# Optimization experiments

Measured on AMD Instinct MI355X. Metric: run time of the kernel, lower is better.

## Reference

```python
import jax, jax.numpy as jnp
import numpy as np

NUM_EXPERTS = 8
K = 2
N_EMBD = 1024
HIDDEN = 4 * N_EMBD
BATCH = 2
SEQ = 1024
LB_SCALE = 0.01
NOISY_STD = 1.0
INIT_S = 0.02


def setup_inputs() -> dict:
    key = jax.random.key(0)
    ks = jax.random.split(key, 8)
    D, H, E = N_EMBD, HIDDEN, NUM_EXPERTS
    return {
        "x": jax.random.normal(ks[0], (BATCH, SEQ, D), jnp.float32),
        "noise": jax.random.normal(ks[1], (BATCH, SEQ, E), jnp.float32),  # torch.randn_like(logits)
        "gate_w": jax.random.normal(ks[2], (E, D), jnp.float32) * INIT_S,
        "noise_weight": jnp.zeros((E,), jnp.float32),  # initialized to zeros in the module
        "w1": jax.random.normal(ks[3], (E, H, D), jnp.float32) * INIT_S,
        "b1": jnp.zeros((E, H), jnp.float32),
        "w2": jax.random.normal(ks[4], (E, H, D), jnp.float32) * INIT_S,
        "b2": jnp.zeros((E, H), jnp.float32),
        "wp": jax.random.normal(ks[5], (E, D, H), jnp.float32) * INIT_S,
        "bp": jnp.zeros((E, D), jnp.float32),
    }


def reference(x, noise, gate_w, noise_weight, w1, b1, w2, b2, wp, bp):
    B, S, D = x.shape
    E = gate_w.shape[0]

    # ---- TopKGateParallel ----
    logits = jnp.einsum('bsd,ed->bse', x, gate_w)           # [B,S,E]
    gate_weights = jax.nn.softmax(logits, axis=-1)
    gw_mean = gate_weights.reshape(-1, E).mean(axis=0)       # [E]
    load_balance_loss = jnp.mean((gw_mean - 1.0 / E) ** 2) * LB_SCALE  # mse vs uniform

    logits_noisy = logits + (noise * NOISY_STD) * noise_weight
    top_v, top_i = jax.lax.top_k(logits_noisy, K)            # [B,S,K]
    # scatter top-k logits into a -inf sea, then softmax -> zeros at non-topk slots
    topk_mask = jnp.sum(jax.nn.one_hot(top_i, E, dtype=jnp.float32), axis=-2) > 0  # [B,S,E]
    sparse_logits = jnp.where(topk_mask, logits_noisy, -jnp.inf)
    top_k_gated_weights = jax.nn.softmax(sparse_logits, axis=-1)  # [B,S,E]

    # ---- expert compute + weighted combine (world_size=1: all experts local) ----
    x_flat = x.reshape(B * S, D)                              # [T,D]
    w_flat = top_k_gated_weights.reshape(B * S, E)            # [T,E]
    y = jnp.zeros_like(x_flat)
    for e in range(E):  # fixed small set of experts
        h = x_flat @ w1[e].T + b1[e]                          # [T,H]
        g = x_flat @ w2[e].T + b2[e]                          # [T,H]
        out_e = (h * jax.nn.silu(g)) @ wp[e].T + bp[e]        # [T,D]
        y = y + w_flat[:, e:e + 1] * out_e
    y = y.reshape(B, S, D)
    return y, load_balance_loss
```

## Files before the change

kernel.cpp:

```cpp
#include <hip/hip_runtime.h>

#define TOK 2048
#define DIM 1024
#define HID 4096
#define NE 8
#define KSPLIT 4
#define TMAX 24

typedef unsigned short u16;
typedef __attribute__((ext_vector_type(8))) short s16x8;
typedef __attribute__((ext_vector_type(4))) float f32x4;

__device__ __forceinline__ u16 f2b(float f) {
  unsigned u = __builtin_bit_cast(unsigned, f);
  unsigned r = (u + 0x7fffu + ((u >> 16) & 1u)) >> 16;
  return (u16)r;
}

__device__ __forceinline__ void gld_lds16(const void* g, void* l) {
  __builtin_amdgcn_global_load_lds((const __attribute__((address_space(1))) void*)g,
                                   (__attribute__((address_space(3))) void*)l, 16, 0, 0);
}

__global__ __launch_bounds__(256) void k_gate(const float* __restrict__ x,
    const float* __restrict__ noise, const float* __restrict__ gw,
    const float* __restrict__ nw,
    int* __restrict__ tok_e, float* __restrict__ tok_w,
    int* __restrict__ bhist, float* __restrict__ bgw, u16* __restrict__ x16) {
  const int wid = threadIdx.x >> 6, lane = threadIdx.x & 63;
  const int t = blockIdx.x * 4 + wid;
  const float* xr = x + (size_t)t * DIM + lane * 16;
  float acc[NE];
#pragma unroll
  for (int e = 0; e < NE; ++e) acc[e] = 0.f;
  u16 xb[16];
#pragma unroll
  for (int j = 0; j < 4; ++j) {
    float4 xv = *(const float4*)(xr + j * 4);
    xb[j * 4 + 0] = f2b(xv.x); xb[j * 4 + 1] = f2b(xv.y);
    xb[j * 4 + 2] = f2b(xv.z); xb[j * 4 + 3] = f2b(xv.w);
#pragma unroll
    for (int e = 0; e < NE; ++e) {
      float4 gv = *(const float4*)(gw + e * DIM + lane * 16 + j * 4);
      acc[e] += xv.x * gv.x + xv.y * gv.y + xv.z * gv.z + xv.w * gv.w;
    }
  }
  *(s16x8*)(x16 + (size_t)t * DIM + lane * 16) = *(const s16x8*)xb;
  *(s16x8*)(x16 + (size_t)t * DIM + lane * 16 + 8) = *(const s16x8*)(xb + 8);
#pragma unroll
  for (int e = 0; e < NE; ++e) {
#pragma unroll
    for (int off = 32; off >= 1; off >>= 1) acc[e] += __shfl_xor(acc[e], off);
  }
  float m = acc[0];
#pragma unroll
  for (int e = 1; e < NE; ++e) m = fmaxf(m, acc[e]);
  float p[NE]; float s = 0.f;
#pragma unroll
  for (int e = 0; e < NE; ++e) { p[e] = expf(acc[e] - m); s += p[e]; }
  float inv = 1.f / s;
  float v[NE];
#pragma unroll
  for (int e = 0; e < NE; ++e) v[e] = acc[e] + noise[t * NE + e] * nw[e];
  float v0 = -3.4e38f, v1 = -3.4e38f; int i0 = 0, i1 = 0;
#pragma unroll
  for (int e = 0; e < NE; ++e) {
    float ve = v[e];
    if (ve > v0) { v1 = v0; i1 = i0; v0 = ve; i0 = e; }
    else if (ve > v1) { v1 = ve; i1 = e; }
  }
  float e1 = expf(v1 - v0);
  float den = 1.f + e1;
  float w0 = 1.f / den, w1v = e1 / den;

  __shared__ float pl[4][NE];
  __shared__ int el[4][2];
  if (lane == 0) {
#pragma unroll
    for (int e = 0; e < NE; ++e) pl[wid][e] = p[e] * inv;
    el[wid][0] = i0; el[wid][1] = i1;
    tok_e[t * 2] = i0; tok_e[t * 2 + 1] = i1;
    tok_w[t * 2] = w0; tok_w[t * 2 + 1] = w1v;
  }
  __syncthreads();
  if (threadIdx.x < NE) {
    const int e = threadIdx.x;
    float ps = pl[0][e] + pl[1][e] + pl[2][e] + pl[3][e];
    int h = 0;
#pragma unroll
    for (int j = 0; j < 4; ++j) {
      h += (el[j][0] == e);
      h += (el[j][1] == e);
    }
    bgw[blockIdx.x * NE + e] = ps;
    bhist[blockIdx.x * NE + e] = h;
  }
}

__global__ __launch_bounds__(512) void k_scan(const int* __restrict__ bhist,
    const float* __restrict__ bgw, int* __restrict__ blk_off, int* __restrict__ prefix,
    int* __restrict__ counts, int* __restrict__ tile_tab, float* __restrict__ loss_out) {
  const int i = threadIdx.x, lane = i & 63, wv = i >> 6;
  __shared__ int wsum[8];
  __shared__ float wfs[8];
  __shared__ int etot[8];
  __shared__ float fsum[8];
  for (int e = 0; e < NE; ++e) {
    int v = bhist[i * NE + e];
    int sc = v;
#pragma unroll
    for (int off = 1; off < 64; off <<= 1) {
      int u = __shfl_up(sc, off);
      if (lane >= off) sc += u;
    }
    float f = bgw[i * NE + e];
#pragma unroll
    for (int off = 32; off >= 1; off >>= 1) f += __shfl_xor(f, off);
    if (lane == 63) wsum[wv] = sc;
    if (lane == 0) wfs[wv] = f;
    __syncthreads();
    int base = 0;
    for (int w2 = 0; w2 < wv; ++w2) base += wsum[w2];
    blk_off[i * NE + e] = base + sc - v;
    if (i == 0) {
      float tf = 0.f;
      for (int w2 = 0; w2 < 8; ++w2) tf += wfs[w2];
      fsum[e] = tf;
    }
    if (i == 511) etot[e] = base + sc;
    __syncthreads();
  }
  if (i == 0) {
    int sacc = 0;
    float l = 0.f;
    int tt = 0;
#pragma unroll
    for (int e = 0; e < NE; ++e) { prefix[e] = sacc; counts[e] = etot[e]; sacc += etot[e]; }
    for (int e = 0; e < NE; ++e) {
      const int nmt = (etot[e] + 255) >> 8;
      for (int m2 = 0; m2 < nmt; ++m2) tile_tab[tt++] = (e << 16) | m2;
    }
    for (; tt < TMAX; ++tt) tile_tab[tt] = -1;
#pragma unroll
    for (int e = 0; e < NE; ++e) {
      float d = fsum[e] * (1.f / TOK) - 0.125f;
      l += d * d;
    }
    *loss_out = l * (0.01f / NE);
  }
}

__global__ __launch_bounds__(256) void k_build(const int* __restrict__ tok_e,
    const float* __restrict__ tok_w, const int* __restrict__ prefix,
    const int* __restrict__ blk_off, int* __restrict__ ent, float* __restrict__ entw,
    int* __restrict__ inv) {
  const int t = blockIdx.x * 256 + threadIdx.x;
  const int g = t >> 2;
  const int base = (t & 3) * 2;
  int ee[8];
#pragma unroll
  for (int j = 0; j < 8; ++j) ee[j] = tok_e[g * 8 + j];
#pragma unroll
  for (int s = 0; s < 2; ++s) {
    const int e = ee[base + s];
    int rank = 0;
#pragma unroll
    for (int j = 0; j < 8; ++j) rank += (j < base + s) && (ee[j] == e);
    const int idx = prefix[e] + blk_off[g * NE + e] + rank;
    ent[idx] = t * 2 + s;
    entw[idx] = tok_w[t * 2 + s];
    inv[t * 2 + s] = idx;
  }
}

__global__ __launch_bounds__(512) void k_gemm1f(const u16* __restrict__ x16,
    const float* __restrict__ w1, const float* __restrict__ w2,
    const float* __restrict__ b1, const float* __restrict__ b2,
    const int* __restrict__ ent, const int* __restrict__ counts,
    const int* __restrict__ prefix, const int* __restrict__ tile_tab,
    u16* __restrict__ act) {
  const int tt = tile_tab[blockIdx.y];
  if (tt < 0) return;
  const int e = tt >> 16, mt = tt & 0xffff, nt = blockIdx.x;
  const int cnt = counts[e];
  const int pfx = prefix[e];
  const int tid = threadIdx.x, w = tid >> 6, l = tid & 63;

  __shared__ u16 smem[2][16384];

  const int r0 = tid >> 2;
  const int c = (tid & 3) ^ ((tid >> 3) & 3);
  int g0 = mt * 256 + r0;       if (g0 >= cnt) g0 = cnt - 1;
  int g1 = mt * 256 + 128 + r0; if (g1 >= cnt) g1 = cnt - 1;
  const u16* sa0 = x16 + (size_t)(ent[pfx + g0] >> 1) * DIM + c * 8;
  const u16* sa1 = x16 + (size_t)(ent[pfx + g1] >> 1) * DIM + c * 8;
  const float* pB1 = w1 + ((size_t)e * HID + nt * 128 + r0) * DIM + c * 8;
  const float* pB2 = w2 + ((size_t)e * HID + nt * 128 + r0) * DIM + c * 8;
  const int oA0 = tid * 8, oA1 = 4096 + tid * 8;
  const int oB1 = 8192 + tid * 8, oB2 = 12288 + tid * 8;

  const int wr = w >> 1, wc = w & 1;
  const int xs = ((l >> 4) ^ ((l >> 1) & 3)) * 8;
  const int ra = (wr * 64 + (l & 15)) * 32 + xs;
  const int rb = (wc * 64 + (l & 15)) * 32 + xs;

  f32x4 acc1[4][4], acc2[4][4];
#pragma unroll
  for (int m = 0; m < 4; ++m)
#pragma unroll
    for (int n = 0; n < 4; ++n) {
      acc1[m][n] = (f32x4){0.f, 0.f, 0.f, 0.f};
      acc2[m][n] = (f32x4){0.f, 0.f, 0.f, 0.f};
    }

  f32x4 rb0_, rb1_, rb2_, rb3_;
  auto LOADB = [&](int k0) {
    rb0_ = *(const f32x4*)(pB1 + k0);
    rb1_ = *(const f32x4*)(pB1 + k0 + 4);
    rb2_ = *(const f32x4*)(pB2 + k0);
    rb3_ = *(const f32x4*)(pB2 + k0 + 4);
  };
  auto STAGEA = [&](int buf, int k0) {
    gld_lds16(sa0 + k0, &smem[buf][oA0]);
    gld_lds16(sa1 + k0, &smem[buf][oA1]);
  };
  auto WRITEB = [&](int buf) {
    u16 u[16];
    u[0] = f2b(rb0_[0]); u[1] = f2b(rb0_[1]); u[2] = f2b(rb0_[2]); u[3] = f2b(rb0_[3]);
    u[4] = f2b(rb1_[0]); u[5] = f2b(rb1_[1]); u[6] = f2b(rb1_[2]); u[7] = f2b(rb1_[3]);
    u[8] = f2b(rb2_[0]); u[9] = f2b(rb2_[1]); u[10] = f2b(rb2_[2]); u[11] = f2b(rb2_[3]);
    u[12] = f2b(rb3_[0]); u[13] = f2b(rb3_[1]); u[14] = f2b(rb3_[2]); u[15] = f2b(rb3_[3]);
    *(s16x8*)&smem[buf][oB1] = *(const s16x8*)u;
    *(s16x8*)&smem[buf][oB2] = *(const s16x8*)(u + 8);
  };

  const int NT = DIM / 32;
  LOADB(0);
  STAGEA(0, 0);
  asm volatile("s_waitcnt vmcnt(0)" ::: "memory");
  WRITEB(0);
  asm volatile("s_waitcnt lgkmcnt(0)" ::: "memory");
  __builtin_amdgcn_sched_barrier(0);
  __builtin_amdgcn_s_barrier();
  int cur = 0;
  for (int kt = 0; kt < NT; ++kt) {
    if (kt + 1 < NT) { LOADB((kt + 1) * 32); STAGEA(cur ^ 1, (kt + 1) * 32); }
    const u16* S = &smem[cur][0];
    s16x8 af[4];
#pragma unroll
    for (int m = 0; m < 4; ++m) af[m] = *(const s16x8*)(S + ra + m * 512);
#pragma unroll
    for (int n = 0; n < 4; ++n) {
      s16x8 bf1 = *(const s16x8*)(S + 8192 + rb + n * 512);
      s16x8 bf2 = *(const s16x8*)(S + 12288 + rb + n * 512);
#pragma unroll
      for (int m = 0; m < 4; ++m) {
        acc1[m][n] = __builtin_amdgcn_mfma_f32_16x16x32_bf16(af[m], bf1, acc1[m][n], 0, 0, 0);
        acc2[m][n] = __builtin_amdgcn_mfma_f32_16x16x32_bf16(af[m], bf2, acc2[m][n], 0, 0, 0);
      }
    }
    if (kt + 1 < NT) {
      asm volatile("s_waitcnt vmcnt(0)" ::: "memory");
      __builtin_amdgcn_sched_barrier(0);
      WRITEB(cur ^ 1);
      asm volatile("s_waitcnt lgkmcnt(0)" ::: "memory");
      __builtin_amdgcn_sched_barrier(0);
      __builtin_amdgcn_s_barrier();
    }
    cur ^= 1;
  }

#pragma unroll
  for (int n = 0; n < 4; ++n) {
    const int col = nt * 128 + wc * 64 + n * 16 + (l & 15);
    const float bb1 = b1[(size_t)e * HID + col];
    const float bb2 = b2[(size_t)e * HID + col];
#pragma unroll
    for (int m = 0; m < 4; ++m) {
#pragma unroll
      for (int r = 0; r < 4; ++r) {
        const int row = mt * 256 + wr * 64 + m * 16 + (l >> 4) * 4 + r;
        if (row < cnt) {
          float h = acc1[m][n][r] + bb1;
          float g = acc2[m][n][r] + bb2;
          float a = h * g / (1.f + expf(-g));
          act[(size_t)(pfx + row) * HID + col] = f2b(a);
        }
      }
    }
  }
}

__global__ __launch_bounds__(512) void k_gemm2f(const u16* __restrict__ act,
    const float* __restrict__ wp, const float* __restrict__ bp,
    const float* __restrict__ entw, const int* __restrict__ counts,
    const int* __restrict__ prefix, const int* __restrict__ tile_tab,
    float* __restrict__ yp) {
  const int tt = tile_tab[blockIdx.y];
  if (tt < 0) return;
  const int e = tt >> 16, mt = tt & 0xffff;
  const int sk = blockIdx.z, nt = blockIdx.x;
  const int cnt = counts[e];
  const int pfx = prefix[e];
  const int tid = threadIdx.x, w = tid >> 6, l = tid & 63;

  __shared__ u16 smem[2][16384];

  const int r0 = tid >> 2;
  const int c = (tid & 3) ^ ((tid >> 3) & 3);
  int g0 = mt * 256 + r0;       if (g0 >= cnt) g0 = cnt - 1;
  int g1 = mt * 256 + 128 + r0; if (g1 >= cnt) g1 = cnt - 1;
  const int kbase = sk * (HID / KSPLIT);
  const u16* sa0 = act + (size_t)(pfx + g0) * HID + kbase + c * 8;
  const u16* sa1 = act + (size_t)(pfx + g1) * HID + kbase + c * 8;
  const float* pB0 = wp + ((size_t)e * DIM + nt * 256 + r0) * HID + kbase + c * 8;
  const float* pB1h = pB0 + (size_t)128 * HID;
  const int oA0 = tid * 8, oA1 = 4096 + tid * 8;
  const int oB0 = 8192 + tid * 8, oB1 = 12288 + tid * 8;

  const int wr = w >> 2, wc = w & 3;
  const int xs = ((l >> 4) ^ ((l >> 1) & 3)) * 8;
  const int ra = (wr * 128 + (l & 15)) * 32 + xs;
  const int rb = 8192 + (wc * 64 + (l & 15)) * 32 + xs;

  f32x4 acc[8][4];
#pragma unroll
  for (int m = 0; m < 8; ++m)
#pragma unroll
    for (int n = 0; n < 4; ++n) acc[m][n] = (f32x4){0.f, 0.f, 0.f, 0.f};

  f32x4 rb0_, rb1_, rb2_, rb3_;
  auto LOADB = [&](int k0) {
    rb0_ = *(const f32x4*)(pB0 + k0);
    rb1_ = *(const f32x4*)(pB0 + k0 + 4);
    rb2_ = *(const f32x4*)(pB1h + k0);
    rb3_ = *(const f32x4*)(pB1h + k0 + 4);
  };
  auto STAGEA = [&](int buf, int k0) {
    gld_lds16(sa0 + k0, &smem[buf][oA0]);
    gld_lds16(sa1 + k0, &smem[buf][oA1]);
  };
  auto WRITEB = [&](int buf) {
    u16 u[16];
    u[0] = f2b(rb0_[0]); u[1] = f2b(rb0_[1]); u[2] = f2b(rb0_[2]); u[3] = f2b(rb0_[3]);
    u[4] = f2b(rb1_[0]); u[5] = f2b(rb1_[1]); u[6] = f2b(rb1_[2]); u[7] = f2b(rb1_[3]);
    u[8] = f2b(rb2_[0]); u[9] = f2b(rb2_[1]); u[10] = f2b(rb2_[2]); u[11] = f2b(rb2_[3]);
    u[12] = f2b(rb3_[0]); u[13] = f2b(rb3_[1]); u[14] = f2b(rb3_[2]); u[15] = f2b(rb3_[3]);
    *(s16x8*)&smem[buf][oB0] = *(const s16x8*)u;
    *(s16x8*)&smem[buf][oB1] = *(const s16x8*)(u + 8);
  };

  const int NIT = HID / KSPLIT / 32;
  LOADB(0);
  STAGEA(0, 0);
  asm volatile("s_waitcnt vmcnt(0)" ::: "memory");
  WRITEB(0);
  asm volatile("s_waitcnt lgkmcnt(0)" ::: "memory");
  __builtin_amdgcn_sched_barrier(0);
  __builtin_amdgcn_s_barrier();
  int cur = 0;
  for (int kt = 0; kt < NIT; ++kt) {
    if (kt + 1 < NIT) { LOADB((kt + 1) * 32); STAGEA(cur ^ 1, (kt + 1) * 32); }
    const u16* S = &smem[cur][0];
#pragma unroll
    for (int n = 0; n < 4; ++n) {
      s16x8 bf = *(const s16x8*)(S + rb + n * 512);
#pragma unroll
      for (int m = 0; m < 8; ++m) {
        s16x8 af = *(const s16x8*)(S + ra + m * 512);
        acc[m][n] = __builtin_amdgcn_mfma_f32_16x16x32_bf16(af, bf, acc[m][n], 0, 0, 0);
      }
    }
    if (kt + 1 < NIT) {
      asm volatile("s_waitcnt vmcnt(0)" ::: "memory");
      __builtin_amdgcn_sched_barrier(0);
      WRITEB(cur ^ 1);
      asm volatile("s_waitcnt lgkmcnt(0)" ::: "memory");
      __builtin_amdgcn_sched_barrier(0);
      __builtin_amdgcn_s_barrier();
    }
    cur ^= 1;
  }

#pragma unroll
  for (int n = 0; n < 4; ++n) {
    const int col = nt * 256 + wc * 64 + n * 16 + (l & 15);
    const float bpv = (sk == 0) ? bp[(size_t)e * DIM + col] : 0.f;
#pragma unroll
    for (int m = 0; m < 8; ++m) {
#pragma unroll
      for (int r = 0; r < 4; ++r) {
        const int row = mt * 256 + wr * 128 + m * 16 + (l >> 4) * 4 + r;
        if (row < cnt) {
          const int idx = pfx + row;
          yp[((size_t)sk * (TOK * 2) + idx) * DIM + col] = entw[idx] * (acc[m][n][r] + bpv);
        }
      }
    }
  }
}

__global__ __launch_bounds__(256) void k_final(const float* __restrict__ yp,
    const int* __restrict__ inv, float* __restrict__ out) {
  const int t = blockIdx.x;
  const int d = threadIdx.x * 4;
  const int i0 = inv[t * 2], i1 = inv[t * 2 + 1];
  float4 s = {0.f, 0.f, 0.f, 0.f};
#pragma unroll
  for (int sk = 0; sk < KSPLIT; ++sk) {
    float4 a = *(const float4*)(yp + ((size_t)sk * (TOK * 2) + i0) * DIM + d);
    float4 b = *(const float4*)(yp + ((size_t)sk * (TOK * 2) + i1) * DIM + d);
    s.x += a.x + b.x; s.y += a.y + b.y; s.z += a.z + b.z; s.w += a.w + b.w;
  }
  *(float4*)(out + (size_t)t * DIM + d) = s;
}

extern "C" void kernel_launch(void* const* d_in, const int* in_sizes, int n_in,
                              void* d_out, int out_size, void* d_ws, size_t ws_size,
                              hipStream_t stream) {
  const float* x      = (const float*)d_in[0];
  const float* noise  = (const float*)d_in[1];
  const float* gate_w = (const float*)d_in[2];
  const float* nw     = (const float*)d_in[3];
  const float* w1     = (const float*)d_in[4];
  const float* b1     = (const float*)d_in[5];
  const float* w2     = (const float*)d_in[6];
  const float* b2     = (const float*)d_in[7];
  const float* wp     = (const float*)d_in[8];
  const float* bp     = (const float*)d_in[9];
  float* out = (float*)d_out;
  char* ws = (char*)d_ws;

  const size_t SZ_X16 = (size_t)TOK * DIM * 2;
  const size_t SZ_ACT = (size_t)TOK * 2 * HID * 2;
  const size_t SZ_YP  = (size_t)KSPLIT * TOK * 2 * DIM * 4;

  u16* x16  = (u16*)ws;
  u16* act  = (u16*)(ws + SZ_X16);
  float* yp = (float*)(ws + SZ_X16 + SZ_ACT);
  char* meta = ws + SZ_X16 + SZ_ACT + SZ_YP;
  int*   tok_e    = (int*)(meta);
  float* tok_w    = (float*)(meta + 16384);
  int*   ent      = (int*)(meta + 32768);
  float* entw     = (float*)(meta + 49152);
  int*   bhist    = (int*)(meta + 65536);
  float* bgw      = (float*)(meta + 81920);
  int*   blk_off  = (int*)(meta + 98304);
  int*   inv      = (int*)(meta + 114688);
  int*   counts   = (int*)(meta + 131072);
  int*   prefix   = (int*)(meta + 131072 + 64);
  int*   tile_tab = (int*)(meta + 131072 + 128);

  k_gate<<<TOK / 4, 256, 0, stream>>>(x, noise, gate_w, nw, tok_e, tok_w, bhist, bgw, x16);
  k_scan<<<1, 512, 0, stream>>>(bhist, bgw, blk_off, prefix, counts, tile_tab,
                                out + (size_t)TOK * DIM);
  k_build<<<TOK / 256, 256, 0, stream>>>(tok_e, tok_w, prefix, blk_off, ent, entw, inv);
  k_gemm1f<<<dim3(HID / 128, TMAX), 512, 0, stream>>>(x16, w1, w2, b1, b2, ent,
                                                      counts, prefix, tile_tab, act);
  k_gemm2f<<<dim3(DIM / 256, TMAX, KSPLIT), 512, 0, stream>>>(act, wp, bp, entw,
                                                              counts, prefix, tile_tab, yp);
  k_final<<<TOK, 256, 0, stream>>>(yp, inv, out);
}
```

Measured before the change: 366.6 us.

## Deepen B-operand prefetch to two stages with partial vmcnt waits in expert GEMMs

Both expert GEMM kernels now keep two register sets for the fp32 B-weight tiles, so global loads for tile k+2 are in flight while tile k is computed. The loop is unrolled by two, and full vmcnt(0) waits become vmcnt(4) so the newest loads stay outstanding. This hides more global-load latency behind the MFMA work. The cost is more VGPRs, an extra barrier per step, and delicate waitcnt accounting that could race if the count is wrong.

Result: faster. 330.4 us (-9.9%).

```diff
diff --git a/kernel.cpp b/kernel.cpp
--- a/kernel.cpp
+++ b/kernel.cpp
@@ -213,38 +213,30 @@
       acc2[m][n] = (f32x4){0.f, 0.f, 0.f, 0.f};
     }
 
-  f32x4 rb0_, rb1_, rb2_, rb3_;
-  auto LOADB = [&](int k0) {
-    rb0_ = *(const f32x4*)(pB1 + k0);
-    rb1_ = *(const f32x4*)(pB1 + k0 + 4);
-    rb2_ = *(const f32x4*)(pB2 + k0);
-    rb3_ = *(const f32x4*)(pB2 + k0 + 4);
+  f32x4 a0_, a1_, a2_, a3_;
+  f32x4 b0_, b1_, b2_, b3_;
+
+  auto LOADB = [&](f32x4& r0_, f32x4& r1_, f32x4& r2_, f32x4& r3_, int k0) {
+    r0_ = *(const f32x4*)(pB1 + k0);
+    r1_ = *(const f32x4*)(pB1 + k0 + 4);
+    r2_ = *(const f32x4*)(pB2 + k0);
+    r3_ = *(const f32x4*)(pB2 + k0 + 4);
   };
   auto STAGEA = [&](int buf, int k0) {
     gld_lds16(sa0 + k0, &smem[buf][oA0]);
     gld_lds16(sa1 + k0, &smem[buf][oA1]);
   };
-  auto WRITEB = [&](int buf) {
+  auto WRITEB = [&](int buf, const f32x4& r0_, const f32x4& r1_,
+                    const f32x4& r2_, const f32x4& r3_) {
     u16 u[16];
-    u[0] = f2b(rb0_[0]); u[1] = f2b(rb0_[1]); u[2] = f2b(rb0_[2]); u[3] = f2b(rb0_[3]);
-    u[4] = f2b(rb1_[0]); u[5] = f2b(rb1_[1]); u[6] = f2b(rb1_[2]); u[7] = f2b(rb1_[3]);
-    u[8] = f2b(rb2_[0]); u[9] = f2b(rb2_[1]); u[10] = f2b(rb2_[2]); u[11] = f2b(rb2_[3]);
-    u[12] = f2b(rb3_[0]); u[13] = f2b(rb3_[1]); u[14] = f2b(rb3_[2]); u[15] = f2b(rb3_[3]);
+    u[0] = f2b(r0_[0]); u[1] = f2b(r0_[1]); u[2] = f2b(r0_[2]); u[3] = f2b(r0_[3]);
+    u[4] = f2b(r1_[0]); u[5] = f2b(r1_[1]); u[6] = f2b(r1_[2]); u[7] = f2b(r1_[3]);
+    u[8] = f2b(r2_[0]); u[9] = f2b(r2_[1]); u[10] = f2b(r2_[2]); u[11] = f2b(r2_[3]);
+    u[12] = f2b(r3_[0]); u[13] = f2b(r3_[1]); u[14] = f2b(r3_[2]); u[15] = f2b(r3_[3]);
     *(s16x8*)&smem[buf][oB1] = *(const s16x8*)u;
     *(s16x8*)&smem[buf][oB2] = *(const s16x8*)(u + 8);
   };
-
-  const int NT = DIM / 32;
-  LOADB(0);
-  STAGEA(0, 0);
-  asm volatile("s_waitcnt vmcnt(0)" ::: "memory");
-  WRITEB(0);
-  asm volatile("s_waitcnt lgkmcnt(0)" ::: "memory");
-  __builtin_amdgcn_sched_barrier(0);
-  __builtin_amdgcn_s_barrier();
-  int cur = 0;
-  for (int kt = 0; kt < NT; ++kt) {
-    if (kt + 1 < NT) { LOADB((kt + 1) * 32); STAGEA(cur ^ 1, (kt + 1) * 32); }
+  auto MSTEP = [&](int cur) {
     const u16* S = &smem[cur][0];
     s16x8 af[4];
 #pragma unroll
@@ -259,15 +251,45 @@
         acc2[m][n] = __builtin_amdgcn_mfma_f32_16x16x32_bf16(af[m], bf2, acc2[m][n], 0, 0, 0);
       }
     }
-    if (kt + 1 < NT) {
-      asm volatile("s_waitcnt vmcnt(0)" ::: "memory");
+  };
+
+  const int NT = DIM / 32;
+  LOADB(a0_, a1_, a2_, a3_, 0);
+  STAGEA(0, 0);
+  LOADB(b0_, b1_, b2_, b3_, 32);
+  asm volatile("s_waitcnt vmcnt(4)" ::: "memory");
+  __builtin_amdgcn_sched_barrier(0);
+  WRITEB(0, a0_, a1_, a2_, a3_);
+  STAGEA(1, 32);
+  asm volatile("s_waitcnt lgkmcnt(0)" ::: "memory");
+  __builtin_amdgcn_sched_barrier(0);
+  __builtin_amdgcn_s_barrier();
+
+  for (int kt = 0; kt < NT; kt += 2) {
+    if (kt + 2 < NT) LOADB(a0_, a1_, a2_, a3_, (kt + 2) * 32);
+    MSTEP(0);
+    __builtin_amdgcn_s_barrier();
+    if (kt + 2 < NT) asm volatile("s_waitcnt vmcnt(4)" ::: "memory");
+    else             asm volatile("s_waitcnt vmcnt(0)" ::: "memory");
+    __builtin_amdgcn_sched_barrier(0);
+    WRITEB(1, b0_, b1_, b2_, b3_);
+    if (kt + 2 < NT) STAGEA(0, (kt + 2) * 32);
+    asm volatile("s_waitcnt lgkmcnt(0)" ::: "memory");
+    __builtin_amdgcn_sched_barrier(0);
+    __builtin_amdgcn_s_barrier();
+    if (kt + 3 < NT) LOADB(b0_, b1_, b2_, b3_, (kt + 3) * 32);
+    MSTEP(1);
+    if (kt + 2 < NT) {
+      __builtin_amdgcn_s_barrier();
+      if (kt + 3 < NT) asm volatile("s_waitcnt vmcnt(4)" ::: "memory");
+      else             asm volatile("s_waitcnt vmcnt(0)" ::: "memory");
       __builtin_amdgcn_sched_barrier(0);
-      WRITEB(cur ^ 1);
+      WRITEB(0, a0_, a1_, a2_, a3_);
+      if (kt + 3 < NT) STAGEA(1, (kt + 3) * 32);
       asm volatile("s_waitcnt lgkmcnt(0)" ::: "memory");
       __builtin_amdgcn_sched_barrier(0);
       __builtin_amdgcn_s_barrier();
     }
-    cur ^= 1;
   }
 
 #pragma unroll
@@ -329,38 +351,30 @@
 #pragma unroll
     for (int n = 0; n < 4; ++n) acc[m][n] = (f32x4){0.f, 0.f, 0.f, 0.f};
 
-  f32x4 rb0_, rb1_, rb2_, rb3_;
-  auto LOADB = [&](int k0) {
-    rb0_ = *(const f32x4*)(pB0 + k0);
-    rb1_ = *(const f32x4*)(pB0 + k0 + 4);
-    rb2_ = *(const f32x4*)(pB1h + k0);
-    rb3_ = *(const f32x4*)(pB1h + k0 + 4);
+  f32x4 a0_, a1_, a2_, a3_;
+  f32x4 b0_, b1_, b2_, b3_;
+
+  auto LOADB = [&](f32x4& r0_, f32x4& r1_, f32x4& r2_, f32x4& r3_, int k0) {
+    r0_ = *(const f32x4*)(pB0 + k0);
+    r1_ = *(const f32x4*)(pB0 + k0 + 4);
+    r2_ = *(const f32x4*)(pB1h + k0);
+    r3_ = *(const f32x4*)(pB1h + k0 + 4);
   };
   auto STAGEA = [&](int buf, int k0) {
     gld_lds16(sa0 + k0, &smem[buf][oA0]);
     gld_lds16(sa1 + k0, &smem[buf][oA1]);
   };
-  auto WRITEB = [&](int buf) {
+  auto WRITEB = [&](int buf, const f32x4& r0_, const f32x4& r1_,
+                    const f32x4& r2_, const f32x4& r3_) {
     u16 u[16];
-    u[0] = f2b(rb0_[0]); u[1] = f2b(rb0_[1]); u[2] = f2b(rb0_[2]); u[3] = f2b(rb0_[3]);
-    u[4] = f2b(rb1_[0]); u[5] = f2b(rb1_[1]); u[6] = f2b(rb1_[2]); u[7] = f2b(rb1_[3]);
-    u[8] = f2b(rb2_[0]); u[9] = f2b(rb2_[1]); u[10] = f2b(rb2_[2]); u[11] = f2b(rb2_[3]);
-    u[12] = f2b(rb3_[0]); u[13] = f2b(rb3_[1]); u[14] = f2b(rb3_[2]); u[15] = f2b(rb3_[3]);
+    u[0] = f2b(r0_[0]); u[1] = f2b(r0_[1]); u[2] = f2b(r0_[2]); u[3] = f2b(r0_[3]);
+    u[4] = f2b(r1_[0]); u[5] = f2b(r1_[1]); u[6] = f2b(r1_[2]); u[7] = f2b(r1_[3]);
+    u[8] = f2b(r2_[0]); u[9] = f2b(r2_[1]); u[10] = f2b(r2_[2]); u[11] = f2b(r2_[3]);
+    u[12] = f2b(r3_[0]); u[13] = f2b(r3_[1]); u[14] = f2b(r3_[2]); u[15] = f2b(r3_[3]);
     *(s16x8*)&smem[buf][oB0] = *(const s16x8*)u;
     *(s16x8*)&smem[buf][oB1] = *(const s16x8*)(u + 8);
   };
-
-  const int NIT = HID / KSPLIT / 32;
-  LOADB(0);
-  STAGEA(0, 0);
-  asm volatile("s_waitcnt vmcnt(0)" ::: "memory");
-  WRITEB(0);
-  asm volatile("s_waitcnt lgkmcnt(0)" ::: "memory");
-  __builtin_amdgcn_sched_barrier(0);
-  __builtin_amdgcn_s_barrier();
-  int cur = 0;
-  for (int kt = 0; kt < NIT; ++kt) {
-    if (kt + 1 < NIT) { LOADB((kt + 1) * 32); STAGEA(cur ^ 1, (kt + 1) * 32); }
+  auto MSTEP = [&](int cur) {
     const u16* S = &smem[cur][0];
 #pragma unroll
     for (int n = 0; n < 4; ++n) {
@@ -371,15 +385,45 @@
         acc[m][n] = __builtin_amdgcn_mfma_f32_16x16x32_bf16(af, bf, acc[m][n], 0, 0, 0);
       }
     }
-    if (kt + 1 < NIT) {
-      asm volatile("s_waitcnt vmcnt(0)" ::: "memory");
+  };
+
+  const int NIT = HID / KSPLIT / 32;
+  LOADB(a0_, a1_, a2_, a3_, 0);
+  STAGEA(0, 0);
+  LOADB(b0_, b1_, b2_, b3_, 32);
+  asm volatile("s_waitcnt vmcnt(4)" ::: "memory");
+  __builtin_amdgcn_sched_barrier(0);
+  WRITEB(0, a0_, a1_, a2_, a3_);
+  STAGEA(1, 32);
+  asm volatile("s_waitcnt lgkmcnt(0)" ::: "memory");
+  __builtin_amdgcn_sched_barrier(0);
+  __builtin_amdgcn_s_barrier();
+
+  for (int kt = 0; kt < NIT; kt += 2) {
+    if (kt + 2 < NIT) LOADB(a0_, a1_, a2_, a3_, (kt + 2) * 32);
+    MSTEP(0);
+    __builtin_amdgcn_s_barrier();
+    if (kt + 2 < NIT) asm volatile("s_waitcnt vmcnt(4)" ::: "memory");
+    else              asm volatile("s_waitcnt vmcnt(0)" ::: "memory");
+    __builtin_amdgcn_sched_barrier(0);
+    WRITEB(1, b0_, b1_, b2_, b3_);
+    if (kt + 2 < NIT) STAGEA(0, (kt + 2) * 32);
+    asm volatile("s_waitcnt lgkmcnt(0)" ::: "memory");
+    __builtin_amdgcn_sched_barrier(0);
+    __builtin_amdgcn_s_barrier();
+    if (kt + 3 < NIT) LOADB(b0_, b1_, b2_, b3_, (kt + 3) * 32);
+    MSTEP(1);
+    if (kt + 2 < NIT) {
+      __builtin_amdgcn_s_barrier();
+      if (kt + 3 < NIT) asm volatile("s_waitcnt vmcnt(4)" ::: "memory");
+      else              asm volatile("s_waitcnt vmcnt(0)" ::: "memory");
       __builtin_amdgcn_sched_barrier(0);
-      WRITEB(cur ^ 1);
+      WRITEB(0, a0_, a1_, a2_, a3_);
+      if (kt + 3 < NIT) STAGEA(1, (kt + 3) * 32);
       asm volatile("s_waitcnt lgkmcnt(0)" ::: "memory");
       __builtin_amdgcn_sched_barrier(0);
       __builtin_amdgcn_s_barrier();
     }
-    cur ^= 1;
   }
 
 #pragma unroll
```
